# Kernel optimization log

Measured on AMD Instinct MI355X. Metric: run time of the kernel, lower is better.

Reference implementation:

```python
import jax, jax.numpy as jnp
import numpy as np

N_CLASSES = 1000
FEAT_DIM = 256
N = 65536


def setup_inputs() -> dict:
    key = jax.random.key(0)
    k1, k2, k3 = jax.random.split(key, 3)
    gt = jax.random.randint(k1, (N, N_CLASSES), 0, 2, dtype=jnp.int32)
    features = jax.random.normal(k2, (N, FEAT_DIM), dtype=jnp.float32)
    centers = jax.random.normal(k3, (N_CLASSES, FEAT_DIM), dtype=jnp.float32)
    return {"gt": gt, "features": features, "centers": centers}


def reference(gt, features, centers):
    # loss = (1/N) * sum_c sum_{i : gt[i,c] > 0} ||features[i] - centers[c]||^2
    # Vectorized via ||f||^2 + ||c||^2 - 2 f.c  (replaces the per-class python loop)
    mask = (gt > 0).astype(features.dtype)                      # [N, C]
    f_sq = jnp.sum(features * features, axis=1)                 # [N]
    c_sq = jnp.sum(centers * centers, axis=1)                   # [C]
    cross = features @ centers.T                                # [N, C]
    dist = f_sq[:, None] + c_sq[None, :] - 2.0 * cross          # [N, C]
    num_instances = features.shape[0]
    return jnp.sum(mask * dist) / num_instances
```

## Files before the change

kernel.cpp:

```cpp
#include <hip/hip_runtime.h>
#include <stdint.h>

#define N_ROWS 65536
#define N_CLS  1000
#define KPAD   1024
#define FEAT   256
#define MT     64
#define BK     64
#define NIT    (KPAD/BK)
#define LDA    72

typedef short bf16x8 __attribute__((ext_vector_type(8)));
typedef float f32x4  __attribute__((ext_vector_type(4)));

__device__ __forceinline__ ushort f32_to_bf16_rne(float f) {
    union { float f; uint32_t u; } x; x.f = f;
    uint32_t u = x.u + 0x7FFFu + ((x.u >> 16) & 1u);
    return (ushort)(u >> 16);
}

__global__ __launch_bounds__(256) void prep_kernel(const float* __restrict__ centers,
                                                   ushort* __restrict__ Bfrag,
                                                   float* __restrict__ csq,
                                                   float* __restrict__ out) {
    const int c = blockIdx.x;
    const int n = threadIdx.x;
    float v = 0.f;
    if (c < N_CLS) v = centers[(size_t)c * FEAT + n];

    const int it   = c >> 6;
    const int ks   = (c >> 5) & 1;
    const int quad = (c >> 3) & 3;
    const int j    = c & 7;
    const int w    = n >> 6;
    const int nt   = (n >> 4) & 3;
    const int ml   = n & 15;
    const int lane = quad * 16 + ml;
    const size_t idx = ((size_t)(((it * 2 + ks) * 4 + w) * 4 + nt) * 64 + lane) * 8 + j;
    Bfrag[idx] = f32_to_bf16_rne(v);

    float sq = v * v;
    #pragma unroll
    for (int off = 32; off > 0; off >>= 1) sq += __shfl_down(sq, off);
    __shared__ float red[4];
    if ((threadIdx.x & 63) == 0) red[threadIdx.x >> 6] = sq;
    __syncthreads();
    if (threadIdx.x == 0) {
        csq[c] = red[0] + red[1] + red[2] + red[3];
        if (c == 0) out[0] = 0.f;
    }
}

__global__ __launch_bounds__(256, 4) void main_kernel(const int* __restrict__ gt,
                                                      const float* __restrict__ features,
                                                      const ushort* __restrict__ Bfrag,
                                                      const float* __restrict__ csq,
                                                      float* __restrict__ out) {
    __shared__ ushort As[2 * MT * LDA];
    __shared__ float  rcS[256];
    __shared__ float  t2S[256];
    __shared__ float  rowcnt[MT];
    __shared__ float  t2row[MT];
    __shared__ float  blockred[4];

    const int tid  = threadIdx.x;
    const int m0   = blockIdx.x * MT;
    const int r    = tid >> 2;
    const int kc   = tid & 3;
    const int lane = tid & 63;
    const int w    = tid >> 6;
    const int ml   = lane & 15;
    const int quad = lane >> 4;

    f32x4 acc[4][4];
    #pragma unroll
    for (int i = 0; i < 4; i++)
        #pragma unroll
        for (int j = 0; j < 4; j++)
            #pragma unroll
            for (int k = 0; k < 4; k++) acc[i][j][k] = 0.f;

    int   rci = 0;
    float t2  = 0.f;
    const int* gtrow = gt + (size_t)(m0 + r) * N_CLS;

    auto load_gt = [&](int it, int (&vv)[16]) {
        const int kb = it * BK + kc * 16;
        if (kb + 16 <= N_CLS) {
            const int4* p = (const int4*)(gtrow + kb);
            int4 a0 = p[0], a1 = p[1], a2 = p[2], a3 = p[3];
            vv[0]=a0.x;  vv[1]=a0.y;  vv[2]=a0.z;  vv[3]=a0.w;
            vv[4]=a1.x;  vv[5]=a1.y;  vv[6]=a1.z;  vv[7]=a1.w;
            vv[8]=a2.x;  vv[9]=a2.y;  vv[10]=a2.z; vv[11]=a2.w;
            vv[12]=a3.x; vv[13]=a3.y; vv[14]=a3.z; vv[15]=a3.w;
        } else {
            #pragma unroll
            for (int j = 0; j < 16; j++) {
                int k = kb + j;
                vv[j] = (k < N_CLS) ? gtrow[k] : 0;
            }
        }
    };

    auto convert_store = [&](int buf, int it, const int (&vv)[16]) {
        const int kb = it * BK + kc * 16;
        const float4* cp = (const float4*)(csq + kb);
        float4 q0 = cp[0], q1 = cp[1], q2 = cp[2], q3 = cp[3];
        float cs[16] = {q0.x,q0.y,q0.z,q0.w, q1.x,q1.y,q1.z,q1.w,
                        q2.x,q2.y,q2.z,q2.w, q3.x,q3.y,q3.z,q3.w};
        uint32_t u[8];
        #pragma unroll
        for (int j = 0; j < 8; j++)
            u[j] = (uint32_t)(vv[2*j] + (vv[2*j+1] << 16)) * 0x3F80u;
        #pragma unroll
        for (int j = 0; j < 16; j++) {
            rci += vv[j];
            t2  += (float)vv[j] * cs[j];
        }
        uint4* dst = (uint4*)&As[buf * (MT * LDA) + r * LDA + kc * 16];
        dst[0] = make_uint4(u[0], u[1], u[2], u[3]);
        dst[1] = make_uint4(u[4], u[5], u[6], u[7]);
    };

    {
        int v0[16];
        load_gt(0, v0);
        convert_store(0, 0, v0);
    }
    __syncthreads();

    int cur = 0;
    const ushort* bbase = Bfrag + ((size_t)w * 4) * 64 * 8 + (size_t)lane * 8;

    for (int it = 0; it < NIT; ++it) {
        const bool hn = (it + 1 < NIT);

        bf16x8 b0[4], b1[4];
        {
            const ushort* p0 = bbase + (size_t)(it * 2 + 0) * (4 * 4 * 64 * 8);
            const ushort* p1 = bbase + (size_t)(it * 2 + 1) * (4 * 4 * 64 * 8);
            #pragma unroll
            for (int nt = 0; nt < 4; ++nt) b0[nt] = *(const bf16x8*)(p0 + nt * 64 * 8);
            #pragma unroll
            for (int nt = 0; nt < 4; ++nt) b1[nt] = *(const bf16x8*)(p1 + nt * 64 * 8);
        }

        int vn[16];
        if (hn) load_gt(it + 1, vn);

        const ushort* Ab = &As[cur * (MT * LDA)];
        #pragma unroll
        for (int ks = 0; ks < 2; ++ks) {
            const int kk = ks * 32 + quad * 8;
            bf16x8 af[4];
            #pragma unroll
            for (int mt = 0; mt < 4; mt++)
                af[mt] = *(const bf16x8*)&Ab[(mt * 16 + ml) * LDA + kk];
            #pragma unroll
            for (int mt = 0; mt < 4; mt++)
                #pragma unroll
                for (int nt = 0; nt < 4; nt++)
                    acc[mt][nt] = __builtin_amdgcn_mfma_f32_16x16x32_bf16(
                        af[mt], ks ? b1[nt] : b0[nt], acc[mt][nt], 0, 0, 0);
        }

        if (hn) convert_store(cur ^ 1, it + 1, vn);
        __syncthreads();
        cur ^= 1;
    }

    rcS[tid] = (float)rci;
    t2S[tid] = t2;
    __syncthreads();
    if (tid < MT) {
        rowcnt[tid] = rcS[tid*4] + rcS[tid*4+1] + rcS[tid*4+2] + rcS[tid*4+3];
        t2row[tid]  = t2S[tid*4] + t2S[tid*4+1] + t2S[tid*4+2] + t2S[tid*4+3];
    }
    __syncthreads();

    float part = 0.f;
    #pragma unroll
    for (int mt = 0; mt < 4; mt++) {
        #pragma unroll
        for (int nt = 0; nt < 4; nt++) {
            const int n = w * 64 + nt * 16 + ml;
            #pragma unroll
            for (int reg = 0; reg < 4; reg++) {
                const int ri = mt * 16 + quad * 4 + reg;
                const float f = features[(size_t)(m0 + ri) * FEAT + n];
                const float T = acc[mt][nt][reg];
                part += f * (rowcnt[ri] * f - 2.f * T) + t2row[ri] * (1.f / 256.f);
            }
        }
    }
    #pragma unroll
    for (int off = 32; off > 0; off >>= 1) part += __shfl_down(part, off);
    if (lane == 0) blockred[w] = part;
    __syncthreads();
    if (tid == 0)
        atomicAdd(out, (blockred[0] + blockred[1] + blockred[2] + blockred[3]) *
                           (1.f / (float)N_ROWS));
}

extern "C" void kernel_launch(void* const* d_in, const int* in_sizes, int n_in,
                              void* d_out, int out_size, void* d_ws, size_t ws_size,
                              hipStream_t stream) {
    const int*   gt       = (const int*)d_in[0];
    const float* features = (const float*)d_in[1];
    const float* centers  = (const float*)d_in[2];
    float*       out      = (float*)d_out;

    ushort* Bfrag = (ushort*)d_ws;
    float*  csq   = (float*)((char*)d_ws + (size_t)FEAT * KPAD * 2);

    prep_kernel<<<KPAD, 256, 0, stream>>>(centers, Bfrag, csq, out);
    main_kernel<<<N_ROWS / MT, 256, 0, stream>>>(gt, features, Bfrag, csq, out);
}
```

Before: 435.3 us.

## Load gt directly into MFMA A-fragments in registers, drop LDS staging

The gt mask tile is no longer staged through double-buffered shared memory. Each lane now loads the gt elements that match its own MFMA A-fragment layout straight from global memory and converts them to bf16 in registers, using a two-stage software pipeline with no per-iteration barriers. The row tile is halved to 32 rows, and row counts and the c_sq term are reduced with shuffles, with csq cached in LDS. In exchange each lane issues narrower 32-byte row-strided global loads that coalesce less well, there are twice as many blocks, and each wave loads redundant B fragments at a lower MFMA-to-load ratio.

```diff
diff --git a/kernel.cpp b/kernel.cpp
--- a/kernel.cpp
+++ b/kernel.cpp
@@ -5,10 +5,8 @@
 #define N_CLS  1000
 #define KPAD   1024
 #define FEAT   256
-#define MT     64
-#define BK     64
-#define NIT    (KPAD/BK)
-#define LDA    72
+#define MT     32
+#define NSTG   32
 
 typedef short bf16x8 __attribute__((ext_vector_type(8)));
 typedef float f32x4  __attribute__((ext_vector_type(4)));
@@ -28,15 +26,14 @@
     float v = 0.f;
     if (c < N_CLS) v = centers[(size_t)c * FEAT + n];
 
-    const int it   = c >> 6;
-    const int ks   = (c >> 5) & 1;
+    const int s    = c >> 5;
     const int quad = (c >> 3) & 3;
     const int j    = c & 7;
     const int w    = n >> 6;
     const int nt   = (n >> 4) & 3;
     const int ml   = n & 15;
     const int lane = quad * 16 + ml;
-    const size_t idx = ((size_t)(((it * 2 + ks) * 4 + w) * 4 + nt) * 64 + lane) * 8 + j;
+    const size_t idx = (((size_t)(s * 4 + w) * 4 + nt) * 64 + lane) * 8 + j;
     Bfrag[idx] = f32_to_bf16_rne(v);
 
     float sq = v * v;
@@ -51,151 +48,136 @@
     }
 }
 
-__global__ __launch_bounds__(256, 4) void main_kernel(const int* __restrict__ gt,
+__global__ __launch_bounds__(256, 3) void main_kernel(const int* __restrict__ gt,
                                                       const float* __restrict__ features,
                                                       const ushort* __restrict__ Bfrag,
                                                       const float* __restrict__ csq,
                                                       float* __restrict__ out) {
-    __shared__ ushort As[2 * MT * LDA];
-    __shared__ float  rcS[256];
-    __shared__ float  t2S[256];
-    __shared__ float  rowcnt[MT];
-    __shared__ float  t2row[MT];
-    __shared__ float  blockred[4];
+    __shared__ float csqS[KPAD];
+    __shared__ float blockred[4];
 
     const int tid  = threadIdx.x;
-    const int m0   = blockIdx.x * MT;
-    const int r    = tid >> 2;
-    const int kc   = tid & 3;
     const int lane = tid & 63;
     const int w    = tid >> 6;
     const int ml   = lane & 15;
     const int quad = lane >> 4;
-
-    f32x4 acc[4][4];
-    #pragma unroll
-    for (int i = 0; i < 4; i++)
+    const int m0   = blockIdx.x * MT;
+
+    *(float4*)&csqS[tid * 4] = *(const float4*)&csq[tid * 4];
+
+    f32x4 acc[2][4];
+    #pragma unroll
+    for (int i = 0; i < 2; i++)
         #pragma unroll
         for (int j = 0; j < 4; j++)
             #pragma unroll
             for (int k = 0; k < 4; k++) acc[i][j][k] = 0.f;
 
-    int   rci = 0;
-    float t2  = 0.f;
-    const int* gtrow = gt + (size_t)(m0 + r) * N_CLS;
-
-    auto load_gt = [&](int it, int (&vv)[16]) {
-        const int kb = it * BK + kc * 16;
-        if (kb + 16 <= N_CLS) {
-            const int4* p = (const int4*)(gtrow + kb);
-            int4 a0 = p[0], a1 = p[1], a2 = p[2], a3 = p[3];
-            vv[0]=a0.x;  vv[1]=a0.y;  vv[2]=a0.z;  vv[3]=a0.w;
-            vv[4]=a1.x;  vv[5]=a1.y;  vv[6]=a1.z;  vv[7]=a1.w;
-            vv[8]=a2.x;  vv[9]=a2.y;  vv[10]=a2.z; vv[11]=a2.w;
-            vv[12]=a3.x; vv[13]=a3.y; vv[14]=a3.z; vv[15]=a3.w;
+    const int qoff = quad * 8;
+    const int* g0 = gt + (size_t)(m0 + ml) * N_CLS;
+    const int* g1 = gt + (size_t)(m0 + 16 + ml) * N_CLS;
+
+    auto ld_gt = [&](int s, int4 (&d)[4]) {
+        const int k = s * 32 + qoff;
+        if (k < N_CLS) {
+            d[0] = *(const int4*)(g0 + k);
+            d[1] = *(const int4*)(g0 + k + 4);
+            d[2] = *(const int4*)(g1 + k);
+            d[3] = *(const int4*)(g1 + k + 4);
         } else {
+            d[0] = d[1] = d[2] = d[3] = make_int4(0, 0, 0, 0);
+        }
+    };
+
+    const ushort* bb = Bfrag + ((size_t)w * 4 * 64 + lane) * 8;
+    auto ld_B = [&](int s, bf16x8 (&b)[4]) {
+        const ushort* p = bb + (size_t)s * 8192;
+        b[0] = *(const bf16x8*)(p);
+        b[1] = *(const bf16x8*)(p + 512);
+        b[2] = *(const bf16x8*)(p + 1024);
+        b[3] = *(const bf16x8*)(p + 1536);
+    };
+
+    int   rci0 = 0, rci1 = 0;
+    float t2 = 0.f;
+
+    auto convert = [&](int s, const int4 (&d)[4], bf16x8 (&a)[2]) {
+        const int k = s * 32 + qoff;
+        float4 c0 = *(const float4*)&csqS[k];
+        float4 c1 = *(const float4*)&csqS[k + 4];
+        int v0[8] = {d[0].x, d[0].y, d[0].z, d[0].w, d[1].x, d[1].y, d[1].z, d[1].w};
+        int v1[8] = {d[2].x, d[2].y, d[2].z, d[2].w, d[3].x, d[3].y, d[3].z, d[3].w};
+        union { uint32_t u[4]; bf16x8 v; } p0, p1;
+        #pragma unroll
+        for (int j = 0; j < 4; j++) {
+            p0.u[j] = (uint32_t)(v0[2*j] + (v0[2*j+1] << 16)) * 0x3F80u;
+            p1.u[j] = (uint32_t)(v1[2*j] + (v1[2*j+1] << 16)) * 0x3F80u;
+        }
+        a[0] = p0.v;
+        a[1] = p1.v;
+        float cs[8] = {c0.x, c0.y, c0.z, c0.w, c1.x, c1.y, c1.z, c1.w};
+        #pragma unroll
+        for (int j = 0; j < 8; j++) {
+            rci0 += v0[j];
+            rci1 += v1[j];
+            t2   += cs[j] * (float)(v0[j] + v1[j]);
+        }
+    };
+
+    auto domfma = [&](const bf16x8 (&a)[2], const bf16x8 (&b)[4]) {
+        #pragma unroll
+        for (int mt = 0; mt < 2; mt++)
             #pragma unroll
-            for (int j = 0; j < 16; j++) {
-                int k = kb + j;
-                vv[j] = (k < N_CLS) ? gtrow[k] : 0;
-            }
-        }
-    };
-
-    auto convert_store = [&](int buf, int it, const int (&vv)[16]) {
-        const int kb = it * BK + kc * 16;
-        const float4* cp = (const float4*)(csq + kb);
-        float4 q0 = cp[0], q1 = cp[1], q2 = cp[2], q3 = cp[3];
-        float cs[16] = {q0.x,q0.y,q0.z,q0.w, q1.x,q1.y,q1.z,q1.w,
-                        q2.x,q2.y,q2.z,q2.w, q3.x,q3.y,q3.z,q3.w};
-        uint32_t u[8];
-        #pragma unroll
-        for (int j = 0; j < 8; j++)
-            u[j] = (uint32_t)(vv[2*j] + (vv[2*j+1] << 16)) * 0x3F80u;
-        #pragma unroll
-        for (int j = 0; j < 16; j++) {
-            rci += vv[j];
-            t2  += (float)vv[j] * cs[j];
-        }
-        uint4* dst = (uint4*)&As[buf * (MT * LDA) + r * LDA + kc * 16];
-        dst[0] = make_uint4(u[0], u[1], u[2], u[3]);
-        dst[1] = make_uint4(u[4], u[5], u[6], u[7]);
-    };
-
-    {
-        int v0[16];
-        load_gt(0, v0);
-        convert_store(0, 0, v0);
+            for (int nt = 0; nt < 4; nt++)
+                acc[mt][nt] = __builtin_amdgcn_mfma_f32_16x16x32_bf16(
+                    a[mt], b[nt], acc[mt][nt], 0, 0, 0);
+    };
+
+    int4   gtP[4], gtQ[4];
+    bf16x8 BfP[4], BfQ[4], AbfP[2], AbfQ[2];
+    ld_gt(0, gtP);
+    ld_gt(1, gtQ);
+    ld_B(0, BfP);
+    ld_B(1, BfQ);
+    __syncthreads();
+    convert(0, gtP, AbfP);
+
+    for (int s = 0; s < NSTG; s += 2) {
+        const bool hn = (s + 2 < NSTG);
+        if (hn) ld_gt(s + 2, gtP);
+        domfma(AbfP, BfP);
+        convert(s + 1, gtQ, AbfQ);
+        if (hn) ld_B(s + 2, BfP);
+        if (hn) ld_gt(s + 3, gtQ);
+        domfma(AbfQ, BfQ);
+        if (hn) convert(s + 2, gtP, AbfP);
+        if (hn) ld_B(s + 3, BfQ);
     }
-    __syncthreads();
-
-    int cur = 0;
-    const ushort* bbase = Bfrag + ((size_t)w * 4) * 64 * 8 + (size_t)lane * 8;
-
-    for (int it = 0; it < NIT; ++it) {
-        const bool hn = (it + 1 < NIT);
-
-        bf16x8 b0[4], b1[4];
-        {
-            const ushort* p0 = bbase + (size_t)(it * 2 + 0) * (4 * 4 * 64 * 8);
-            const ushort* p1 = bbase + (size_t)(it * 2 + 1) * (4 * 4 * 64 * 8);
-            #pragma unroll
-            for (int nt = 0; nt < 4; ++nt) b0[nt] = *(const bf16x8*)(p0 + nt * 64 * 8);
-            #pragma unroll
-            for (int nt = 0; nt < 4; ++nt) b1[nt] = *(const bf16x8*)(p1 + nt * 64 * 8);
-        }
-
-        int vn[16];
-        if (hn) load_gt(it + 1, vn);
-
-        const ushort* Ab = &As[cur * (MT * LDA)];
-        #pragma unroll
-        for (int ks = 0; ks < 2; ++ks) {
-            const int kk = ks * 32 + quad * 8;
-            bf16x8 af[4];
-            #pragma unroll
-            for (int mt = 0; mt < 4; mt++)
-                af[mt] = *(const bf16x8*)&Ab[(mt * 16 + ml) * LDA + kk];
-            #pragma unroll
-            for (int mt = 0; mt < 4; mt++)
-                #pragma unroll
-                for (int nt = 0; nt < 4; nt++)
-                    acc[mt][nt] = __builtin_amdgcn_mfma_f32_16x16x32_bf16(
-                        af[mt], ks ? b1[nt] : b0[nt], acc[mt][nt], 0, 0, 0);
-        }
-
-        if (hn) convert_store(cur ^ 1, it + 1, vn);
-        __syncthreads();
-        cur ^= 1;
-    }
-
-    rcS[tid] = (float)rci;
-    t2S[tid] = t2;
-    __syncthreads();
-    if (tid < MT) {
-        rowcnt[tid] = rcS[tid*4] + rcS[tid*4+1] + rcS[tid*4+2] + rcS[tid*4+3];
-        t2row[tid]  = t2S[tid*4] + t2S[tid*4+1] + t2S[tid*4+2] + t2S[tid*4+3];
-    }
-    __syncthreads();
+
+    float rc0 = (float)rci0, rc1 = (float)rci1;
+    rc0 += __shfl_xor(rc0, 16); rc0 += __shfl_xor(rc0, 32);
+    rc1 += __shfl_xor(rc1, 16); rc1 += __shfl_xor(rc1, 32);
+    #pragma unroll
+    for (int off = 32; off > 0; off >>= 1) t2 += __shfl_xor(t2, off);
 
     float part = 0.f;
     #pragma unroll
-    for (int mt = 0; mt < 4; mt++) {
+    for (int mt = 0; mt < 2; mt++) {
         #pragma unroll
         for (int nt = 0; nt < 4; nt++) {
             const int n = w * 64 + nt * 16 + ml;
             #pragma unroll
             for (int reg = 0; reg < 4; reg++) {
                 const int ri = mt * 16 + quad * 4 + reg;
+                const float rowcnt = __shfl(mt == 0 ? rc0 : rc1, quad * 4 + reg);
                 const float f = features[(size_t)(m0 + ri) * FEAT + n];
-                const float T = acc[mt][nt][reg];
-                part += f * (rowcnt[ri] * f - 2.f * T) + t2row[ri] * (1.f / 256.f);
+                part += f * (rowcnt * f - 2.f * acc[mt][nt][reg]);
             }
         }
     }
     #pragma unroll
     for (int off = 32; off > 0; off >>= 1) part += __shfl_down(part, off);
-    if (lane == 0) blockred[w] = part;
+    if (lane == 0) blockred[w] = part + (w == 0 ? t2 : 0.f);
     __syncthreads();
     if (tid == 0)
         atomicAdd(out, (blockred[0] + blockred[1] + blockred[2] + blockred[3]) *
```

Measured after the change: 480.1 us. 10.3% more time.
